# Kernel optimization log

Hardware: AMD Instinct MI355X
Metric: run time of the kernel (lower is better)

## Reference

```python
import jax, jax.numpy as jnp
import numpy as np

B, H, S, DK = 2, 16, 2048, 64

def setup_inputs() -> dict:
    key = jax.random.key(0)
    kq, kk, kv, km = jax.random.split(key, 4)
    queries = jax.random.normal(kq, (B, H, S, DK), dtype=jnp.float32)
    keys = jax.random.normal(kk, (B, H, S, DK), dtype=jnp.float32)
    values = jax.random.normal(kv, (B, H, S, DK), dtype=jnp.float32)
    mask = jax.random.randint(km, (B, S, S), 0, 2, dtype=jnp.int32)
    return {"queries": queries, "keys": keys, "values": values, "mask": mask}

def reference(queries, keys, values, mask):
    d_k = queries.shape[-1]
    scale = 1.0 / np.sqrt(d_k).astype(np.float32)
    # [B,H,S,S]
    scores = jnp.einsum('bhqd,bhkd->bhqk', queries, keys) * scale
    m = mask[:, None, :, :]  # broadcast over heads, like mask.unsqueeze(1)
    scores = jnp.where(m == 0, jnp.asarray(-1e9, scores.dtype), scores)
    attn = jax.nn.softmax(scores, axis=-1)
    return jnp.einsum('bhqk,bhkd->bhqd', attn, values)
```

## Files before the change

kernel.cpp:

```cpp
#include <hip/hip_runtime.h>


#define S_   2048
#define D_   64
#define H_   16
#define B_   2
#define BH_  32
#define KVB  64
#define NKV  (S_/KVB)
#define QPB  128
#define NQT  (S_/QPB)

#define KSCALE 0.18033688f

typedef __attribute__((ext_vector_type(8))) _Float16 f16x8;
typedef __attribute__((ext_vector_type(4))) _Float16 f16x4;
typedef __attribute__((ext_vector_type(2))) _Float16 f16x2;
typedef __attribute__((ext_vector_type(4))) float    f32x4;

static __device__ __forceinline__ void async16(const void* g, void* l) {
  __builtin_amdgcn_global_load_lds(
      (const __attribute__((address_space(1))) void*)g,
      (__attribute__((address_space(3))) void*)l, 16, 0, 0);
}

static __device__ __forceinline__ f16x2 pkrtz(float a, float b) {
  return __builtin_bit_cast(f16x2, __builtin_amdgcn_cvt_pkrtz(a, b));
}

__global__ __launch_bounds__(256) void prepass_k(
    const float* __restrict__ K, const float* __restrict__ V,
    const int* __restrict__ M,
    _Float16* __restrict__ Kh, _Float16* __restrict__ Vth,
    unsigned long long* __restrict__ Mb) {
  __shared__ float tile[64][65];
  const int bidx = blockIdx.x;
  const int tid = threadIdx.x;
  if (bidx < 1024) {
    int st = bidx & 31;
    int bh = bidx >> 5;
    const float* src = V + ((size_t)bh * S_ + st * 64) * D_;
    int r = tid >> 2, cq = tid & 3;
#pragma unroll
    for (int j = 0; j < 4; ++j) {
      float4 v = ((const float4*)(src + (size_t)r * D_))[cq + 4 * j];
      int col = (cq + 4 * j) * 4;
      tile[r][col + 0] = v.x; tile[r][col + 1] = v.y;
      tile[r][col + 2] = v.z; tile[r][col + 3] = v.w;
    }
    __syncthreads();
    int d = tid >> 2, s = (tid & 3) * 16;
    _Float16 tmp[16];
#pragma unroll
    for (int j = 0; j < 16; ++j) tmp[j] = (_Float16)tile[s + j][d];
    _Float16* dstp = Vth + ((size_t)bh * D_ + d) * S_ + st * 64 + s;
    *(f16x8*)(dstp)     = *((f16x8*)tmp);
    *(f16x8*)(dstp + 8) = *((f16x8*)tmp + 1);
  } else if (bidx < 1536) {
    int idx = (bidx - 1024) * 256 + tid;
#pragma unroll
    for (int j = 0; j < 8; ++j) {
      int i = idx + j * 131072;
      float4 v = ((const float4*)K)[i];
      f16x4 o = {(_Float16)(v.x * KSCALE), (_Float16)(v.y * KSCALE),
                 (_Float16)(v.z * KSCALE), (_Float16)(v.w * KSCALE)};
      *(f16x4*)(Kh + 4 * (size_t)i) = o;
    }
  } else {
    int lane = tid & 63;
    int wb = (bidx - 1536) * 256 + (tid >> 6) * 64;
    for (int i = 0; i < 64; ++i) {
      int w = wb + i;
      int m = M[(size_t)w * 64 + lane];
      unsigned long long bal = __ballot(m != 0);
      if (lane == 0) Mb[w] = bal;
    }
  }
}

__global__ __launch_bounds__(512, 4) void attn_fwd(
    const float* __restrict__ Qf, const _Float16* __restrict__ Kh,
    const _Float16* __restrict__ Vth, const unsigned long long* __restrict__ Mb,
    float* __restrict__ Out) {
  __shared__ _Float16 Kt[KVB * D_];
  __shared__ _Float16 Vt[D_ * KVB];
  __shared__ _Float16 Pl[8][16 * KVB];
  __shared__ unsigned long long MLUT[16];

  const int tid = threadIdx.x;
  const int lane = tid & 63;
  const int wid = tid >> 6;
  const int g = lane >> 4;
  const int c = lane & 15;
  const int c7 = c & 7;

  if (tid < 16) {
    unsigned w0 = ((tid & 1) ? 0x3C00u : 0u) | ((tid & 2) ? 0x3C000000u : 0u);
    unsigned w1 = ((tid & 4) ? 0x3C00u : 0u) | ((tid & 8) ? 0x3C000000u : 0u);
    MLUT[tid] = (unsigned long long)w0 | ((unsigned long long)w1 << 32);
  }

  int bid = blockIdx.x;
  bid = (bid & 7) * 64 + (bid >> 3);
  const int qt = bid & (NQT - 1);
  const int bh = bid >> 4;
  const int b = bh >> 4;

  const int q0 = qt * QPB + wid * 16;

  f16x8 qf[2];
  {
    const float* qp = Qf + ((size_t)bh * S_ + q0 + c) * D_ + 8 * g;
    _Float16 t[16];
#pragma unroll
    for (int j = 0; j < 8; ++j) t[j] = (_Float16)qp[j];
#pragma unroll
    for (int j = 0; j < 8; ++j) t[8 + j] = (_Float16)qp[32 + j];
    qf[0] = *(f16x8*)t;
    qf[1] = *((f16x8*)t + 1);
  }

  f32x4 accO[4];
#pragma unroll
  for (int dp = 0; dp < 4; ++dp) accO[dp] = {0.f, 0.f, 0.f, 0.f};
  float m_run = -INFINITY, l_run = 0.f;

  const int srow = tid >> 3, sgr = tid & 7;
  const _Float16* kp = Kh + (size_t)bh * S_ * D_ + (size_t)srow * D_ + ((sgr ^ (srow & 7)) << 3);
  const _Float16* vp = Vth + (size_t)bh * D_ * S_ + (size_t)srow * S_ + ((sgr ^ (srow & 7)) << 3);
  _Float16* ldk = &Kt[(tid & ~63) * 8];
  _Float16* ldv = &Vt[(tid & ~63) * 8];
  const unsigned long long* pmb = Mb + ((size_t)b * S_ + q0 + c) * NKV;

  const f16x2 one2 = {(_Float16)1.0f, (_Float16)1.0f};

  for (int kv = 0; kv < NKV; ++kv) {
    __syncthreads();
    async16(kp, ldk);
    async16(vp, ldv);
    kp += KVB * D_;
    vp += KVB;
    unsigned long long mw = pmb[kv];
    __syncthreads();

    f32x4 st[4];
#pragma unroll
    for (int kt = 0; kt < 4; ++kt) {
      int row = kt * 16 + c;
      f16x8 k0 = *(const f16x8*)(&Kt[row * D_ + (((0 * 4 + g) ^ c7) << 3)]);
      f16x8 k1 = *(const f16x8*)(&Kt[row * D_ + (((1 * 4 + g) ^ c7) << 3)]);
      f32x4 a = {0.f, 0.f, 0.f, 0.f};
      a = __builtin_amdgcn_mfma_f32_16x16x32_f16(k0, qf[0], a, 0, 0, 0);
      a = __builtin_amdgcn_mfma_f32_16x16x32_f16(k1, qf[1], a, 0, 0, 0);
      st[kt] = a;
    }

    float pmax = st[0][0];
#pragma unroll
    for (int kt = 0; kt < 4; ++kt)
#pragma unroll
      for (int r = 0; r < 4; ++r) pmax = fmaxf(pmax, st[kt][r]);
    pmax = fmaxf(pmax, __shfl_xor(pmax, 16));
    pmax = fmaxf(pmax, __shfl_xor(pmax, 32));
    if (!__all(pmax - m_run <= 8.f)) {
      float mn = fmaxf(m_run, pmax);
      float cf = __builtin_amdgcn_exp2f(m_run - mn);
      l_run *= cf;
#pragma unroll
      for (int dp = 0; dp < 4; ++dp) accO[dp] = accO[dp] * cf;
      m_run = mn;
    }

    const unsigned mlo = (unsigned)mw, mhi = (unsigned)(mw >> 32);
    float rs = 0.f;
    f16x2 wv[8];
#pragma unroll
    for (int kt = 0; kt < 4; ++kt) {
      unsigned nib = (((kt < 2) ? mlo : mhi) >> (((kt & 1) << 4) + 4 * g)) & 0xFu;
      unsigned long long lut = MLUT[nib];
      f16x2 m01 = __builtin_bit_cast(f16x2, (unsigned)lut);
      f16x2 m23 = __builtin_bit_cast(f16x2, (unsigned)(lut >> 32));
      f16x2 p01 = pkrtz(__builtin_amdgcn_exp2f(st[kt][0] - m_run),
                        __builtin_amdgcn_exp2f(st[kt][1] - m_run));
      f16x2 p23 = pkrtz(__builtin_amdgcn_exp2f(st[kt][2] - m_run),
                        __builtin_amdgcn_exp2f(st[kt][3] - m_run));
      wv[2 * kt]     = p01 * m01;
      wv[2 * kt + 1] = p23 * m23;
      rs = __builtin_amdgcn_fdot2(wv[2 * kt], one2, rs, false);
      rs = __builtin_amdgcn_fdot2(wv[2 * kt + 1], one2, rs, false);
    }
    rs += __shfl_xor(rs, 16);
    rs += __shfl_xor(rs, 32);
    l_run += rs;

    _Float16* pw = Pl[wid] + c * KVB;
#pragma unroll
    for (int kt = 0; kt < 4; ++kt) {
      int gp = (2 * kt + (g >> 1)) ^ c7;
      uint2 wpair = {__builtin_bit_cast(unsigned, wv[2 * kt]),
                     __builtin_bit_cast(unsigned, wv[2 * kt + 1])};
      *(uint2*)(pw + gp * 8 + (g & 1) * 4) = wpair;
    }
    asm volatile("s_waitcnt lgkmcnt(0)" ::: "memory");
    __builtin_amdgcn_sched_barrier(0);

#pragma unroll
    for (int ks = 0; ks < 2; ++ks) {
      const _Float16* pr = Pl[wid] + c * KVB + (((4 * ks + g) ^ c7) << 3);
      f16x8 pf = *(const f16x8*)pr;
#pragma unroll
      for (int dp = 0; dp < 4; ++dp) {
        int row = dp * 16 + c;
        f16x8 vfr = *(const f16x8*)(&Vt[row * KVB + (((4 * ks + g) ^ c7) << 3)]);
        accO[dp] = __builtin_amdgcn_mfma_f32_16x16x32_f16(vfr, pf, accO[dp], 0, 0, 0);
      }
    }
  }

  float inv = 1.0f / l_run;
  float* op = Out + ((size_t)bh * S_ + q0 + c) * D_;
#pragma unroll
  for (int dp = 0; dp < 4; ++dp) {
    f32x4 o = accO[dp] * inv;
    *(f32x4*)(op + dp * 16 + 4 * g) = o;
  }
}

extern "C" void kernel_launch(void* const* d_in, const int* in_sizes, int n_in,
                              void* d_out, int out_size, void* d_ws, size_t ws_size,
                              hipStream_t stream) {
  const float* Q = (const float*)d_in[0];
  const float* K = (const float*)d_in[1];
  const float* V = (const float*)d_in[2];
  const int*   M = (const int*)d_in[3];
  float* Out = (float*)d_out;

  const size_t NE = (size_t)B_ * H_ * S_ * D_;
  _Float16* Kh  = (_Float16*)d_ws;
  _Float16* Vth = Kh + NE;
  unsigned long long* Mb = (unsigned long long*)(Vth + NE);

  prepass_k<<<2048, 256, 0, stream>>>(K, V, M, Kh, Vth, Mb);
  attn_fwd<<<NQT * BH_, 512, 0, stream>>>(Q, Kh, Vth, Mb, Out);
}
```

Before: 201.6 us.

## Double-buffer K/V tiles in LDS with next-tile prefetch and MFMA priority

Splits the K and V shared-memory tiles into two buffers each. The async global-to-LDS load for tile kv+1 is issued right after the iteration's barrier, so it overlaps with the QK^T, softmax and PV work on tile kv, and the second barrier per iteration is gone. The MFMA sections are wrapped in s_setprio to favour matrix issue. The launch-bounds occupancy hint is raised from 4 to 6. That tighter register budget could cause spills, and the doubled LDS footprint lowers how many blocks fit per CU.

```diff
diff --git a/kernel.cpp b/kernel.cpp
--- a/kernel.cpp
+++ b/kernel.cpp
@@ -78,12 +78,12 @@
   }
 }
 
-__global__ __launch_bounds__(512, 4) void attn_fwd(
+__global__ __launch_bounds__(512, 6) void attn_fwd(
     const float* __restrict__ Qf, const _Float16* __restrict__ Kh,
     const _Float16* __restrict__ Vth, const unsigned long long* __restrict__ Mb,
     float* __restrict__ Out) {
-  __shared__ _Float16 Kt[KVB * D_];
-  __shared__ _Float16 Vt[D_ * KVB];
+  __shared__ _Float16 Kt[2][KVB * D_];
+  __shared__ _Float16 Vt[2][D_ * KVB];
   __shared__ _Float16 Pl[8][16 * KVB];
   __shared__ unsigned long long MLUT[16];
 
@@ -126,34 +126,46 @@
   float m_run = -INFINITY, l_run = 0.f;
 
   const int srow = tid >> 3, sgr = tid & 7;
-  const _Float16* kp = Kh + (size_t)bh * S_ * D_ + (size_t)srow * D_ + ((sgr ^ (srow & 7)) << 3);
-  const _Float16* vp = Vth + (size_t)bh * D_ * S_ + (size_t)srow * S_ + ((sgr ^ (srow & 7)) << 3);
-  _Float16* ldk = &Kt[(tid & ~63) * 8];
-  _Float16* ldv = &Vt[(tid & ~63) * 8];
+  const _Float16* kp0 = Kh + (size_t)bh * S_ * D_ + (size_t)srow * D_ + ((sgr ^ (srow & 7)) << 3);
+  const _Float16* vp0 = Vth + (size_t)bh * D_ * S_ + (size_t)srow * S_ + ((sgr ^ (srow & 7)) << 3);
+  _Float16* ldk = &Kt[0][(tid & ~63) * 8];
+  _Float16* ldv = &Vt[0][(tid & ~63) * 8];
   const unsigned long long* pmb = Mb + ((size_t)b * S_ + q0 + c) * NKV;
 
   const f16x2 one2 = {(_Float16)1.0f, (_Float16)1.0f};
 
+  async16(kp0, ldk);
+  async16(vp0, ldv);
+
+#pragma unroll 2
   for (int kv = 0; kv < NKV; ++kv) {
+    const int cur = kv & 1;
     __syncthreads();
-    async16(kp, ldk);
-    async16(vp, ldv);
-    kp += KVB * D_;
-    vp += KVB;
+
     unsigned long long mw = pmb[kv];
-    __syncthreads();
+
+    if (kv + 1 < NKV) {
+      const int nxt = cur ^ 1;
+      async16(kp0 + (size_t)(kv + 1) * (KVB * D_), ldk + nxt * (KVB * D_));
+      async16(vp0 + (size_t)(kv + 1) * KVB,        ldv + nxt * (D_ * KVB));
+    }
+
+    const _Float16* Ktc = Kt[cur];
+    const _Float16* Vtc = Vt[cur];
 
     f32x4 st[4];
+    __builtin_amdgcn_s_setprio(1);
 #pragma unroll
     for (int kt = 0; kt < 4; ++kt) {
       int row = kt * 16 + c;
-      f16x8 k0 = *(const f16x8*)(&Kt[row * D_ + (((0 * 4 + g) ^ c7) << 3)]);
-      f16x8 k1 = *(const f16x8*)(&Kt[row * D_ + (((1 * 4 + g) ^ c7) << 3)]);
+      f16x8 k0 = *(const f16x8*)(&Ktc[row * D_ + (((0 * 4 + g) ^ c7) << 3)]);
+      f16x8 k1 = *(const f16x8*)(&Ktc[row * D_ + (((1 * 4 + g) ^ c7) << 3)]);
       f32x4 a = {0.f, 0.f, 0.f, 0.f};
       a = __builtin_amdgcn_mfma_f32_16x16x32_f16(k0, qf[0], a, 0, 0, 0);
       a = __builtin_amdgcn_mfma_f32_16x16x32_f16(k1, qf[1], a, 0, 0, 0);
       st[kt] = a;
     }
+    __builtin_amdgcn_s_setprio(0);
 
     float pmax = st[0][0];
 #pragma unroll
@@ -204,6 +216,7 @@
     asm volatile("s_waitcnt lgkmcnt(0)" ::: "memory");
     __builtin_amdgcn_sched_barrier(0);
 
+    __builtin_amdgcn_s_setprio(1);
 #pragma unroll
     for (int ks = 0; ks < 2; ++ks) {
       const _Float16* pr = Pl[wid] + c * KVB + (((4 * ks + g) ^ c7) << 3);
@@ -211,10 +224,11 @@
 #pragma unroll
       for (int dp = 0; dp < 4; ++dp) {
         int row = dp * 16 + c;
-        f16x8 vfr = *(const f16x8*)(&Vt[row * KVB + (((4 * ks + g) ^ c7) << 3)]);
+        f16x8 vfr = *(const f16x8*)(&Vtc[row * KVB + (((4 * ks + g) ^ c7) << 3)]);
         accO[dp] = __builtin_amdgcn_mfma_f32_16x16x32_f16(vfr, pf, accO[dp], 0, 0, 0);
       }
     }
+    __builtin_amdgcn_s_setprio(0);
   }
 
   float inv = 1.0f / l_run;
```

Result: faster. 195.0 us (-3.3%).
